# Kernel optimization log

Measured on AMD Instinct MI355X. Metric: run time of the kernel, lower is better.

## Reference

```python
import jax, jax.numpy as jnp
import numpy as np
import math

H = 16
LN_EPS = 1e-5


def setup_inputs() -> dict:
    key = jax.random.key(0)
    ks = jax.random.split(key, 12)
    D = 1024
    F = T = 2048
    S = 512
    inp = {
        "hidden_states": jax.random.normal(ks[0], (S, D), jnp.float32),
        "fpos": jax.random.randint(ks[1], (F,), 0, 512, jnp.int64 if jax.config.jax_enable_x64 else jnp.int32).astype(jnp.int32),
        "tpos": jax.random.randint(ks[2], (T,), 0, 512, jnp.int32),
        "Wq": jax.random.normal(ks[3], (D, D), jnp.float32) * 0.02,
        "Wk": jax.random.normal(ks[4], (D, D), jnp.float32) * 0.02,
        "Wcb": jax.random.normal(ks[5], (D, H), jnp.float32) * 0.02,
        "Wv": jax.random.normal(ks[6], (D, D), jnp.float32) * 0.02,
        "bv": jnp.zeros((D,), jnp.float32),
        "mixing": jax.random.normal(ks[7], (H, D), jnp.float32) * 0.2,
        "Wd": jax.random.normal(ks[8], (D, D), jnp.float32) * 0.02,
        "bd": jnp.zeros((D,), jnp.float32),
        "ln_gamma": jnp.ones((D,), jnp.float32),
        "ln_beta": jnp.zeros((D,), jnp.float32),
    }
    return inp


def reference(hidden_states, fpos, tpos, Wq, Wk, Wcb, Wv, bv, mixing, Wd, bd, ln_gamma, ln_beta):
    D = hidden_states.shape[-1]
    Dh = D // H
    scale = 1.0 / math.sqrt(D / H)  # attention_head_size = dim_key_query_all / num_heads

    fidx = fpos % 512
    tidx = tpos % 512
    from_seq = hidden_states[fidx]            # [F, D]
    to_seq = hidden_states[tidx]              # [T, D]

    q = from_seq @ Wq                          # [F, D]
    k = to_seq @ Wk                            # [T, D]

    # per-head query mixing: mixed_query[h, f, d] = q[f, d] * mixing[h, d]
    mixed_q = q[None, :, :] * mixing[:, None, :]          # [H, F, D]
    scores = jnp.einsum('hfd,td->hft', mixed_q, k)        # [H, F, T]

    # content bias: [T, H] -> broadcast over queries as [H, 1, T]
    cb = (to_seq @ Wcb).T                                 # [H, T]
    scores = (scores + cb[:, None, :]) * scale

    probs = jax.nn.softmax(scores, axis=-1)               # [H, F, T]

    v = (to_seq @ Wv + bv).reshape(-1, H, Dh).transpose(1, 0, 2)  # [H, T, Dh]
    ctx = jnp.matmul(probs, v)                             # [H, F, Dh]
    ctx = ctx.transpose(1, 0, 2).reshape(-1, D)            # [F, D]

    out = ctx @ Wd + bd                                    # [F, D]
    res = from_seq + out

    mu = jnp.mean(res, axis=-1, keepdims=True)
    var = jnp.var(res, axis=-1, keepdims=True)
    normed = (res - mu) / jnp.sqrt(var + LN_EPS)
    return normed * ln_gamma + ln_beta
```

## Files before the change

kernel.cpp:

```cpp
#include <hip/hip_runtime.h>
#include <stdint.h>
#include <math.h>

typedef float    f32x4 __attribute__((ext_vector_type(4)));
typedef float    f32x2 __attribute__((ext_vector_type(2)));
typedef short    s16x8 __attribute__((ext_vector_type(8)));
typedef short    s16x4 __attribute__((ext_vector_type(4)));
typedef unsigned u32x2 __attribute__((ext_vector_type(2)));

#define SCALE_LOG2E 0.1803368751839806f

__device__ __forceinline__ float bf2f(short s) {
  unsigned u = ((unsigned)(unsigned short)s) << 16;
  return __builtin_bit_cast(float, u);
}
__device__ __forceinline__ short f2bf(float f) {
  unsigned u = __builtin_bit_cast(unsigned, f);
  u = u + 0x7fffu + ((u >> 16) & 1u);
  return (short)(u >> 16);
}
__device__ __forceinline__ unsigned cvtpk(float lo, float hi) {
  unsigned r;
  asm("v_cvt_pk_bf16_f32 %0, %1, %2" : "=v"(r) : "v"(lo), "v"(hi));
  return r;
}
__device__ __forceinline__ void g2l16(const void* g, void* l) {
  __builtin_amdgcn_global_load_lds((const __attribute__((address_space(1))) void*)g,
                                   (__attribute__((address_space(3))) void*)l,
                                   16, 0, 0);
}
#define BARRIER() do { __builtin_amdgcn_s_barrier(); __builtin_amdgcn_sched_barrier(0); } while (0)
#define VMCNT(N)  asm volatile("s_waitcnt vmcnt(" #N ")" ::: "memory")
#define LGKM0()   do { asm volatile("s_waitcnt lgkmcnt(0)" ::: "memory"); __builtin_amdgcn_sched_barrier(0); } while (0)
#define MFMA(a, b, c)  __builtin_amdgcn_mfma_f32_16x16x32_bf16(a, b, c, 0, 0, 0)
#define MFMA8(a, b, c) __builtin_amdgcn_mfma_f32_16x16x32_fp8_fp8(a, b, c, 0, 0, 0)

__device__ __forceinline__ int pi32(int t) {
  return (t & ~31) | ((t & 15) << 1) | ((t >> 4) & 1);
}

__global__ void wtrans_kernel(const float* __restrict__ Wq, const float* __restrict__ Wk,
                              const float* __restrict__ Wv, const float* __restrict__ Wd,
                              short* __restrict__ WqT, short* __restrict__ WkT,
                              short* __restrict__ WvT, short* __restrict__ WdT) {
  __shared__ float tile[64][65];
  const float* src; short* dst;
  switch (blockIdx.z) {
    case 0: src = Wq; dst = WqT; break;
    case 1: src = Wk; dst = WkT; break;
    case 2: src = Wv; dst = WvT; break;
    default: src = Wd; dst = WdT; break;
  }
  int k0 = blockIdx.y * 64;
  int n0 = blockIdx.x * 64;
  int tid = threadIdx.x;
#pragma unroll
  for (int p = 0; p < 4; ++p) {
    int idx = p * 1024 + tid * 4;
    int r = idx >> 6, c = idx & 63;
    f32x4 v = *(const f32x4*)(src + (size_t)(k0 + r) * 1024 + n0 + c);
    tile[r][c + 0] = v[0]; tile[r][c + 1] = v[1];
    tile[r][c + 2] = v[2]; tile[r][c + 3] = v[3];
  }
  __syncthreads();
#pragma unroll
  for (int p = 0; p < 2; ++p) {
    int idx = p * 2048 + tid * 8;
    int r = idx >> 6, c = idx & 63;
    s16x8 o;
#pragma unroll
    for (int i = 0; i < 8; ++i) o[i] = f2bf(tile[c + i][r]);
    *(s16x8*)(dst + (size_t)(n0 + r) * 1024 + k0 + c) = o;
  }
}

__global__ void smallconv_kernel(const float* __restrict__ Wcb, const float* __restrict__ mixing,
                                 short* __restrict__ WcbT, short* __restrict__ mixbf) {
  int idx = blockIdx.x * 256 + threadIdx.x;
  if (idx < 16384) {
    int h = idx >> 10, d = idx & 1023;
    WcbT[idx] = f2bf(Wcb[d * 16 + h]);
  } else {
    int j = idx - 16384;
    mixbf[j] = f2bf(mixing[j] * (SCALE_LOG2E * 64.0f));
  }
}

__global__ void gather_kernel(const float* __restrict__ hidden, const int* __restrict__ fpos,
                              const int* __restrict__ tpos, float* __restrict__ from_f,
                              short* __restrict__ from_bf, short* __restrict__ to_bf) {
  int row = blockIdx.x;
  int c = threadIdx.x * 4;
  if (blockIdx.y == 0) {
    int src = fpos[row] & 511;
    f32x4 v = *(const f32x4*)(hidden + (size_t)src * 1024 + c);
    *(f32x4*)(from_f + (size_t)row * 1024 + c) = v;
    s16x4 o;
#pragma unroll
    for (int i = 0; i < 4; ++i) o[i] = f2bf(v[i]);
    *(s16x4*)(from_bf + (size_t)row * 1024 + c) = o;
  } else {
    int src = tpos[row] & 511;
    f32x4 v = *(const f32x4*)(hidden + (size_t)src * 1024 + c);
    s16x4 o;
#pragma unroll
    for (int i = 0; i < 4; ++i) o[i] = f2bf(v[i]);
    *(s16x4*)(to_bf + (size_t)row * 1024 + c) = o;
  }
}

__global__ __launch_bounds__(256, 2)
void qkv_gemm(const short* __restrict__ from_bf, const short* __restrict__ to_bf,
              const short* __restrict__ WqT, const short* __restrict__ WkT,
              const short* __restrict__ WvT, const float* __restrict__ bv,
              short* __restrict__ q_swz, short* __restrict__ k_swz, short* __restrict__ vTs) {
  __shared__ __align__(16) short As[128][64];
  __shared__ __align__(16) short Bs[128][64];
  int mode = blockIdx.z;
  const short* A = (mode == 0) ? from_bf : to_bf;
  const short* B = (mode == 0) ? WqT : (mode == 1) ? WkT : WvT;
  int m0 = blockIdx.x * 128, n0 = blockIdx.y * 128;
  int tid = threadIdx.x;
  int w = tid >> 6, l = tid & 63;
  int wr = w >> 1, wc = w & 1;
  f32x4 acc[4][4] = {};
  for (int k0 = 0; k0 < 1024; k0 += 64) {
    __syncthreads();
#pragma unroll
    for (int i = 0; i < 4; ++i) {
      int off = i * 4096 + tid * 16;
      int r = off >> 7, cb_ = off & 127;
      g2l16(A + ((size_t)(m0 + r) << 10) + k0 + (cb_ >> 1), (short*)As + (off >> 1));
      g2l16(B + ((size_t)(n0 + r) << 10) + k0 + (cb_ >> 1), (short*)Bs + (off >> 1));
    }
    __syncthreads();
#pragma unroll
    for (int ks = 0; ks < 2; ++ks) {
      s16x8 af[4], bfr[4];
#pragma unroll
      for (int m = 0; m < 4; ++m)
        af[m] = *(const s16x8*)&As[wr * 64 + m * 16 + (l & 15)][ks * 32 + (l >> 4) * 8];
#pragma unroll
      for (int n = 0; n < 4; ++n)
        bfr[n] = *(const s16x8*)&Bs[wc * 64 + n * 16 + (l & 15)][ks * 32 + (l >> 4) * 8];
#pragma unroll
      for (int m = 0; m < 4; ++m)
#pragma unroll
        for (int n = 0; n < 4; ++n)
          acc[m][n] = MFMA(af[m], bfr[n], acc[m][n]);
    }
  }
  int lr = (l >> 4) * 4, lc = l & 15;
#pragma unroll
  for (int m = 0; m < 4; ++m)
#pragma unroll
    for (int n = 0; n < 4; ++n) {
      int row = m0 + wr * 64 + m * 16 + lr;
      int col = n0 + wc * 64 + n * 16 + lc;
      if (mode == 0) {
#pragma unroll
        for (int r = 0; r < 4; ++r) {
          int rr = row + r;
          q_swz[(size_t)rr * 1024 + (col ^ ((rr & 7) << 3))] = f2bf(acc[m][n][r]);
        }
      } else if (mode == 1) {
#pragma unroll
        for (int r = 0; r < 4; ++r) {
          int rr = row + r;
          k_swz[(size_t)rr * 1024 + (col ^ ((rr & 7) << 3))] = f2bf(acc[m][n][r]);
        }
      } else {
        float b = bv[col];
#pragma unroll
        for (int r = 0; r < 4; ++r) {
          int rr = row + r;
          int tsw = pi32(rr) ^ ((col & 7) << 3);
          vTs[(size_t)col * 2048 + tsw] = f2bf(acc[m][n][r] + b);
        }
      }
    }
}

__global__ void k8_kernel(const short* __restrict__ k_swz, unsigned char* __restrict__ k8) {
  int gid = blockIdx.x * 256 + threadIdx.x;
  int row = gid >> 7, c = (gid & 127) * 8;
  s16x8 v = *(const s16x8*)(k_swz + ((size_t)row << 10) + c);
  unsigned lo = 0, hi = 0;
  lo = __builtin_amdgcn_cvt_pk_fp8_f32(bf2f(v[0]) * 4.f, bf2f(v[1]) * 4.f, lo, false);
  lo = __builtin_amdgcn_cvt_pk_fp8_f32(bf2f(v[2]) * 4.f, bf2f(v[3]) * 4.f, lo, true);
  hi = __builtin_amdgcn_cvt_pk_fp8_f32(bf2f(v[4]) * 4.f, bf2f(v[5]) * 4.f, hi, false);
  hi = __builtin_amdgcn_cvt_pk_fp8_f32(bf2f(v[6]) * 4.f, bf2f(v[7]) * 4.f, hi, true);
  u32x2 o; o[0] = lo; o[1] = hi;
  *(u32x2*)(k8 + ((size_t)row << 10) + c) = o;
}

__global__ void qmix8_kernel(const short* __restrict__ q_swz, const short* __restrict__ mixbf,
                             unsigned char* __restrict__ qm8) {
  int f = blockIdx.x, h = blockIdx.y;
  int c = threadIdx.x * 8;
  int fs = (f & 7) << 3;
  s16x8 qv = *(const s16x8*)(q_swz + ((size_t)f << 10) + c);
  s16x8 mv = *(const s16x8*)(mixbf + ((size_t)h << 10) + (c ^ fs));
  float p[8];
#pragma unroll
  for (int i = 0; i < 8; ++i) p[i] = bf2f(qv[i]) * bf2f(mv[i]);
  unsigned lo = 0, hi = 0;
  lo = __builtin_amdgcn_cvt_pk_fp8_f32(p[0], p[1], lo, false);
  lo = __builtin_amdgcn_cvt_pk_fp8_f32(p[2], p[3], lo, true);
  hi = __builtin_amdgcn_cvt_pk_fp8_f32(p[4], p[5], hi, false);
  hi = __builtin_amdgcn_cvt_pk_fp8_f32(p[6], p[7], hi, true);
  u32x2 o; o[0] = lo; o[1] = hi;
  *(u32x2*)(qm8 + (((size_t)h * 2048 + f) << 10) + c) = o;
}

__global__ void cb_kernel(const short* __restrict__ to_bf, const short* __restrict__ WcbT,
                          float* __restrict__ cbv) {
  __shared__ short Wl[16 * 1024];
  int tid = threadIdx.x;
  for (int i = tid; i < 2048; i += 256)
    ((s16x8*)Wl)[i] = ((const s16x8*)WcbT)[i];
  __syncthreads();
  int w = tid >> 6, l = tid & 63;
  int t = blockIdx.x * 4 + w;
  const s16x8* xr = (const s16x8*)(to_bf + ((size_t)t << 10) + l * 16);
  s16x8 x0 = xr[0], x1 = xr[1];
  float xf[16];
#pragma unroll
  for (int i = 0; i < 8; ++i) { xf[i] = bf2f(x0[i]); xf[8 + i] = bf2f(x1[i]); }
#pragma unroll
  for (int h = 0; h < 16; ++h) {
    const s16x8* wr_ = (const s16x8*)(Wl + h * 1024 + l * 16);
    s16x8 w0 = wr_[0], w1 = wr_[1];
    float acc = 0.f;
#pragma unroll
    for (int i = 0; i < 8; ++i) { acc += xf[i] * bf2f(w0[i]); acc += xf[8 + i] * bf2f(w1[i]); }
#pragma unroll
    for (int s = 32; s; s >>= 1) acc += __shfl_xor(acc, s);
    if (l == 0) cbv[(size_t)h * 2048 + t] = acc * SCALE_LOG2E;
  }
}

__global__ __launch_bounds__(512, 4)
void attn_kernel(const unsigned char* __restrict__ qm8, const unsigned char* __restrict__ k8,
                 const short* __restrict__ vTs, const float* __restrict__ cbg,
                 float* __restrict__ ctxp, f32x2* __restrict__ mlb) {
  __shared__ __align__(16) char smem[67584];
  char* qmA = smem;          char* qmB = smem + 16384;
  char* ktA = smem + 32768;  char* ktB = smem + 40960;
  char* vt  = smem + 49152;
  float* cbl = (float*)(smem + 65536);
  const int f0 = blockIdx.x * 256, h = blockIdx.y, ts = blockIdx.z;
  const int tb = ts << 9;
  const int tid = threadIdx.x, w = tid >> 6, l = tid & 63;
  const int lr = l >> 4, lc = l & 15;
  const int swz8 = (lc & 7) << 3;
  cbl[tid & 511] = cbg[h * 2048 + tb + (tid & 511)];
  const unsigned char* qbase = qm8 + (((size_t)h * 2048 + f0) << 10);

#define ISSUE_QK(qmb, ktb, k0e, trow0)                                                      \
  do {                                                                                      \
    _Pragma("unroll") for (int i_ = 0; i_ < 2; ++i_) {                                      \
      int off_ = i_ * 8192 + tid * 16;                                                      \
      g2l16(qbase + ((size_t)(off_ >> 6) << 10) + (k0e) + (off_ & 63), (qmb) + off_);       \
    }                                                                                       \
    {                                                                                       \
      int off_ = tid * 16;                                                                  \
      g2l16(k8 + ((size_t)((trow0) + (off_ >> 6)) << 10) + (k0e) + (off_ & 63),             \
            (ktb) + off_);                                                                  \
    }                                                                                       \
  } while (0)

  ISSUE_QK(qmA, ktA, 0, tb);

  float m_run[8], l_run[8];
#pragma unroll
  for (int s2 = 0; s2 < 8; ++s2) { m_run[s2] = -1e30f; l_run[s2] = 0.f; }
  f32x4 ctx[2][4] = {};

  for (int t0 = 0; t0 < 512; t0 += 128) {
#pragma unroll
    for (int i = 0; i < 2; ++i) {
      int off = i * 8192 + tid * 16;
      g2l16(vTs + (((size_t)(h * 64 + (off >> 8))) << 11) + tb + t0 + ((off & 255) >> 1),
            vt + off);
    }
    f32x4 sacc[2][8] = {};
    for (int c = 0; c < 16; ++c) {
      char* qmb = (c & 1) ? qmB : qmA;
      char* ktb = (c & 1) ? ktB : ktA;
      if (c < 15) {
        ISSUE_QK((c & 1) ? qmA : qmB, (c & 1) ? ktA : ktB, (c + 1) * 64, tb + t0);
      } else if (t0 < 384) {
        ISSUE_QK(qmA, ktA, 0, tb + t0 + 128);
      }
      if (c == 0) { VMCNT(5); }
      else if (c == 15 && t0 == 384) { VMCNT(0); }
      else { VMCNT(3); }
      BARRIER();
#pragma unroll
      for (int ks = 0; ks < 2; ++ks) {
        int xr = (ks * 32 + lr * 8) ^ swz8;
        long af0 = *(const long*)(qmb + ((w * 32 + lc) << 6) + xr);
        long af1 = *(const long*)(qmb + ((w * 32 + 16 + lc) << 6) + xr);
        __builtin_amdgcn_s_setprio(1);
#pragma unroll
        for (int n = 0; n < 8; ++n) {
          long bfr = *(const long*)(ktb + ((n * 16 + lc) << 6) + xr);
          sacc[0][n] = MFMA8(af0, bfr, sacc[0][n]);
          sacc[1][n] = MFMA8(af1, bfr, sacc[1][n]);
        }
        __builtin_amdgcn_s_setprio(0);
      }
      BARRIER();
    }
    float pm[8];
#pragma unroll
    for (int s2 = 0; s2 < 8; ++s2) pm[s2] = -1e30f;
#pragma unroll
    for (int m = 0; m < 2; ++m)
#pragma unroll
      for (int n = 0; n < 8; ++n) {
        float cbv = cbl[t0 + n * 16 + lc];
#pragma unroll
        for (int r = 0; r < 4; ++r) {
          float s = fmaf(sacc[m][n][r], 0.00390625f, cbv);
          sacc[m][n][r] = s;
          pm[m * 4 + r] = fmaxf(pm[m * 4 + r], s);
        }
      }
#pragma unroll
    for (int s_ = 1; s_ < 16; s_ <<= 1)
#pragma unroll
      for (int s2 = 0; s2 < 8; ++s2) pm[s2] = fmaxf(pm[s2], __shfl_xor(pm[s2], s_));
    float tsum[8];
#pragma unroll
    for (int s2 = 0; s2 < 8; ++s2) {
      float mnew = fmaxf(m_run[s2], pm[s2]);
      float corr = exp2f(m_run[s2] - mnew);
      m_run[s2] = mnew; l_run[s2] *= corr; tsum[s2] = 0.f;
      int m = s2 >> 2, r = s2 & 3;
#pragma unroll
      for (int n2 = 0; n2 < 4; ++n2) ctx[m][n2][r] *= corr;
    }
#pragma unroll
    for (int m = 0; m < 2; ++m)
#pragma unroll
      for (int n = 0; n < 8; ++n)
#pragma unroll
        for (int r = 0; r < 4; ++r) {
          float e = exp2f(sacc[m][n][r] - m_run[m * 4 + r]);
          sacc[m][n][r] = e;
          tsum[m * 4 + r] += e;
        }
#pragma unroll
    for (int s_ = 1; s_ < 16; s_ <<= 1)
#pragma unroll
      for (int s2 = 0; s2 < 8; ++s2) tsum[s2] += __shfl_xor(tsum[s2], s_);
#pragma unroll
    for (int s2 = 0; s2 < 8; ++s2) l_run[s2] += tsum[s2];
    char* ptw = qmB + (w << 11);
#pragma unroll
    for (int qq = 0; qq < 4; ++qq) {
      if (qq) { LGKM0(); }
#pragma unroll
      for (int m = 0; m < 2; ++m)
#pragma unroll
        for (int r = 0; r < 4; ++r) {
          int row = m * 16 + lr * 4 + r;
          unsigned pk = cvtpk(sacc[m][2 * qq][r], sacc[m][2 * qq + 1][r]);
          *(unsigned*)(ptw + (row << 6) + ((lc << 2) ^ ((row & 3) << 4))) = pk;
        }
      LGKM0();
      s16x8 paf0 = *(const s16x8*)(ptw + (lc << 6) + ((lr * 16) ^ ((lc & 3) << 4)));
      s16x8 paf1 = *(const s16x8*)(ptw + ((16 + lc) << 6) + ((lr * 16) ^ ((lc & 3) << 4)));
#pragma unroll
      for (int n2 = 0; n2 < 4; ++n2) {
        s16x8 vb = *(const s16x8*)(vt + ((n2 * 16 + lc) << 8) +
                                   ((qq * 64 + lr * 16) ^ ((lc & 7) << 4)));
        ctx[0][n2] = MFMA(paf0, vb, ctx[0][n2]);
        ctx[1][n2] = MFMA(paf1, vb, ctx[1][n2]);
      }
    }
    BARRIER();
  }
  const int pb = (h * 4 + ts) * 2048;
#pragma unroll
  for (int m = 0; m < 2; ++m)
#pragma unroll
    for (int n2 = 0; n2 < 4; ++n2)
#pragma unroll
      for (int r = 0; r < 4; ++r) {
        int f = f0 + w * 32 + m * 16 + lr * 4 + r;
        ctxp[((size_t)(pb + f) << 6) + n2 * 16 + lc] = ctx[m][n2][r];
      }
  if (lc == 0) {
#pragma unroll
    for (int s2 = 0; s2 < 8; ++s2) {
      int f = f0 + w * 32 + (s2 >> 2) * 16 + lr * 4 + (s2 & 3);
      f32x2 v; v[0] = m_run[s2]; v[1] = l_run[s2];
      mlb[pb + f] = v;
    }
  }
#undef ISSUE_QK
}

__global__ void combine_kernel(const float* __restrict__ ctxp, const f32x2* __restrict__ mlb,
                               short* __restrict__ ctx_bf) {
  int f = blockIdx.x, tid = threadIdx.x;
  int h = tid >> 4, d4 = (tid & 15) * 4;
  f32x2 ml[4];
  float mx = -1e30f;
#pragma unroll
  for (int p = 0; p < 4; ++p) {
    ml[p] = mlb[(h * 4 + p) * 2048 + f];
    mx = fmaxf(mx, ml[p][0]);
  }
  float e[4], L = 0.f;
#pragma unroll
  for (int p = 0; p < 4; ++p) { e[p] = exp2f(ml[p][0] - mx); L += ml[p][1] * e[p]; }
  float inv = 1.f / L;
  f32x4 s = {};
#pragma unroll
  for (int p = 0; p < 4; ++p) {
    f32x4 cp = *(const f32x4*)(ctxp + (((size_t)(h * 4 + p) * 2048 + f) << 6) + d4);
#pragma unroll
    for (int i = 0; i < 4; ++i) s[i] += cp[i] * e[p];
  }
  s16x4 o;
#pragma unroll
  for (int i = 0; i < 4; ++i) o[i] = f2bf(s[i] * inv);
  *(s16x4*)(ctx_bf + ((size_t)f << 10) + h * 64 + d4) = o;
}

__global__ __launch_bounds__(256, 2)
void gemm_out(const short* __restrict__ A, const short* __restrict__ B,
              const float* __restrict__ bias, const float* __restrict__ resid,
              float* __restrict__ Cout) {
  __shared__ __align__(16) short As[128][64];
  __shared__ __align__(16) short Bs[128][64];
  int m0 = blockIdx.x * 128, n0 = blockIdx.y * 128;
  int tid = threadIdx.x;
  int w = tid >> 6, l = tid & 63;
  int wr = w >> 1, wc = w & 1;
  f32x4 acc[4][4] = {};
  for (int k0 = 0; k0 < 1024; k0 += 64) {
    __syncthreads();
#pragma unroll
    for (int i = 0; i < 4; ++i) {
      int off = i * 4096 + tid * 16;
      int r = off >> 7, cb_ = off & 127;
      g2l16(A + ((size_t)(m0 + r) << 10) + k0 + (cb_ >> 1), (short*)As + (off >> 1));
      g2l16(B + ((size_t)(n0 + r) << 10) + k0 + (cb_ >> 1), (short*)Bs + (off >> 1));
    }
    __syncthreads();
#pragma unroll
    for (int ks = 0; ks < 2; ++ks) {
      s16x8 af[4], bfr[4];
#pragma unroll
      for (int m = 0; m < 4; ++m)
        af[m] = *(const s16x8*)&As[wr * 64 + m * 16 + (l & 15)][ks * 32 + (l >> 4) * 8];
#pragma unroll
      for (int n = 0; n < 4; ++n)
        bfr[n] = *(const s16x8*)&Bs[wc * 64 + n * 16 + (l & 15)][ks * 32 + (l >> 4) * 8];
#pragma unroll
      for (int m = 0; m < 4; ++m)
#pragma unroll
        for (int n = 0; n < 4; ++n)
          acc[m][n] = MFMA(af[m], bfr[n], acc[m][n]);
    }
  }
  int lr = (l >> 4) * 4, lc = l & 15;
#pragma unroll
  for (int m = 0; m < 4; ++m)
#pragma unroll
    for (int n = 0; n < 4; ++n) {
      int row = m0 + wr * 64 + m * 16 + lr;
      int col = n0 + wc * 64 + n * 16 + lc;
      float b = bias[col];
#pragma unroll
      for (int r = 0; r < 4; ++r)
        Cout[(size_t)(row + r) * 1024 + col] = acc[m][n][r] + b + resid[(size_t)(row + r) * 1024 + col];
    }
}

__global__ void ln_kernel(const float* __restrict__ res, const float* __restrict__ gamma,
                          const float* __restrict__ beta, float* __restrict__ out) {
  int row = blockIdx.x, tid = threadIdx.x;
  f32x4 x = *(const f32x4*)(res + ((size_t)row << 10) + tid * 4);
  float s = x[0] + x[1] + x[2] + x[3];
  float s2 = x[0] * x[0] + x[1] * x[1] + x[2] * x[2] + x[3] * x[3];
#pragma unroll
  for (int m = 1; m < 64; m <<= 1) { s += __shfl_xor(s, m); s2 += __shfl_xor(s2, m); }
  __shared__ float red[8];
  int w = tid >> 6, l = tid & 63;
  if (l == 0) { red[w] = s; red[4 + w] = s2; }
  __syncthreads();
  s = red[0] + red[1] + red[2] + red[3];
  s2 = red[4] + red[5] + red[6] + red[7];
  float mu = s * (1.f / 1024.f);
  float var = s2 * (1.f / 1024.f) - mu * mu;
  float rstd = rsqrtf(var + 1e-5f);
  f32x4 o;
#pragma unroll
  for (int i = 0; i < 4; ++i)
    o[i] = (x[i] - mu) * rstd * gamma[tid * 4 + i] + beta[tid * 4 + i];
  *(f32x4*)(out + ((size_t)row << 10) + tid * 4) = o;
}

extern "C" void kernel_launch(void* const* d_in, const int* in_sizes, int n_in,
                              void* d_out, int out_size, void* d_ws, size_t ws_size,
                              hipStream_t stream) {
  const float* hidden = (const float*)d_in[0];
  const int*   fpos   = (const int*)d_in[1];
  const int*   tpos   = (const int*)d_in[2];
  const float* Wq     = (const float*)d_in[3];
  const float* Wk     = (const float*)d_in[4];
  const float* Wcb    = (const float*)d_in[5];
  const float* Wv     = (const float*)d_in[6];
  const float* bv     = (const float*)d_in[7];
  const float* mixing = (const float*)d_in[8];
  const float* Wd     = (const float*)d_in[9];
  const float* bd     = (const float*)d_in[10];
  const float* gamma  = (const float*)d_in[11];
  const float* beta   = (const float*)d_in[12];

  char* p = (char*)d_ws;
  auto alloc = [&](size_t bytes) { char* r = p; p += (bytes + 255) & ~(size_t)255; return r; };
  float* from_f  = (float*)alloc((size_t)2048 * 1024 * 4);
  short* from_bf = (short*)alloc((size_t)2048 * 1024 * 2);
  short* to_bf   = (short*)alloc((size_t)2048 * 1024 * 2);
  short* WqT     = (short*)alloc((size_t)1024 * 1024 * 2);
  short* WkT     = (short*)alloc((size_t)1024 * 1024 * 2);
  short* WvT     = (short*)alloc((size_t)1024 * 1024 * 2);
  short* WdT     = (short*)alloc((size_t)1024 * 1024 * 2);
  short* WcbT    = (short*)alloc((size_t)16 * 1024 * 2);
  short* mixbf   = (short*)alloc((size_t)16 * 1024 * 2);
  short* q_swz   = (short*)alloc((size_t)2048 * 1024 * 2);
  short* k_swz   = (short*)alloc((size_t)2048 * 1024 * 2);
  short* vTs     = (short*)alloc((size_t)1024 * 2048 * 2);
  unsigned char* k8  = (unsigned char*)alloc((size_t)2048 * 1024);
  unsigned char* qm8 = (unsigned char*)alloc((size_t)16 * 2048 * 1024);
  float* cbb     = (float*)alloc((size_t)16 * 2048 * 4);
  short* ctx_bf  = (short*)alloc((size_t)2048 * 1024 * 2);
  float* ctxp    = (float*)alloc((size_t)64 * 2048 * 64 * 4);
  f32x2* mlb     = (f32x2*)alloc((size_t)64 * 2048 * 8);

  wtrans_kernel<<<dim3(16, 16, 4), 256, 0, stream>>>(Wq, Wk, Wv, Wd, WqT, WkT, WvT, WdT);
  smallconv_kernel<<<128, 256, 0, stream>>>(Wcb, mixing, WcbT, mixbf);
  gather_kernel<<<dim3(2048, 2), 256, 0, stream>>>(hidden, fpos, tpos, from_f, from_bf, to_bf);
  qkv_gemm<<<dim3(16, 8, 3), 256, 0, stream>>>(from_bf, to_bf, WqT, WkT, WvT, bv,
                                               q_swz, k_swz, vTs);
  k8_kernel<<<1024, 256, 0, stream>>>(k_swz, k8);
  cb_kernel<<<512, 256, 0, stream>>>(to_bf, WcbT, cbb);
  qmix8_kernel<<<dim3(2048, 16), 128, 0, stream>>>(q_swz, mixbf, qm8);
  attn_kernel<<<dim3(8, 16, 4), 512, 0, stream>>>(qm8, k8, vTs, cbb, ctxp, mlb);
  combine_kernel<<<2048, 256, 0, stream>>>(ctxp, mlb, ctx_bf);
  gemm_out<<<dim3(16, 8), 256, 0, stream>>>(ctx_bf, WdT, bd, from_f, (float*)d_out);
  ln_kernel<<<2048, 256, 0, stream>>>((float*)d_out, gamma, beta, (float*)d_out);
}
```

Measured before the change: 393.8 us.

## Retile attention to 128-query blocks with 2-way key split and wider K chunks

The attention kernel now processes 128 queries per block (16 per wave) across 2 key splits of 1024 instead of 256 queries across 4 splits of 512. It loads 128-byte K chunks per stage with a new 16-row XOR swizzle, and that swizzle moves into the fp8 conversion kernels. The content bias is read straight into registers instead of staged in shared memory, and the combine step merges only 2 partials. The aim is fewer partial outputs and less combine traffic, with longer MFMA inner loops per barrier, at the cost of more LDS per block and lower occupancy (launch bound 2).

Result: faster. 349.5 us (-11.2%).

```diff
diff --git a/kernel.cpp b/kernel.cpp
--- a/kernel.cpp
+++ b/kernel.cpp
@@ -113,7 +113,7 @@
 void qkv_gemm(const short* __restrict__ from_bf, const short* __restrict__ to_bf,
               const short* __restrict__ WqT, const short* __restrict__ WkT,
               const short* __restrict__ WvT, const float* __restrict__ bv,
-              short* __restrict__ q_swz, short* __restrict__ k_swz, short* __restrict__ vTs) {
+              short* __restrict__ q_bf, short* __restrict__ k_bf, short* __restrict__ vTs) {
   __shared__ __align__(16) short As[128][64];
   __shared__ __align__(16) short Bs[128][64];
   int mode = blockIdx.z;
@@ -159,16 +159,10 @@
       int col = n0 + wc * 64 + n * 16 + lc;
       if (mode == 0) {
 #pragma unroll
-        for (int r = 0; r < 4; ++r) {
-          int rr = row + r;
-          q_swz[(size_t)rr * 1024 + (col ^ ((rr & 7) << 3))] = f2bf(acc[m][n][r]);
-        }
+        for (int r = 0; r < 4; ++r) q_bf[(size_t)(row + r) * 1024 + col] = f2bf(acc[m][n][r]);
       } else if (mode == 1) {
 #pragma unroll
-        for (int r = 0; r < 4; ++r) {
-          int rr = row + r;
-          k_swz[(size_t)rr * 1024 + (col ^ ((rr & 7) << 3))] = f2bf(acc[m][n][r]);
-        }
+        for (int r = 0; r < 4; ++r) k_bf[(size_t)(row + r) * 1024 + col] = f2bf(acc[m][n][r]);
       } else {
         float b = bv[col];
 #pragma unroll
@@ -181,26 +175,25 @@
     }
 }
 
-__global__ void k8_kernel(const short* __restrict__ k_swz, unsigned char* __restrict__ k8) {
+__global__ void k8_kernel(const short* __restrict__ k_bf, unsigned char* __restrict__ k8) {
   int gid = blockIdx.x * 256 + threadIdx.x;
   int row = gid >> 7, c = (gid & 127) * 8;
-  s16x8 v = *(const s16x8*)(k_swz + ((size_t)row << 10) + c);
+  s16x8 v = *(const s16x8*)(k_bf + ((size_t)row << 10) + c);
   unsigned lo = 0, hi = 0;
   lo = __builtin_amdgcn_cvt_pk_fp8_f32(bf2f(v[0]) * 4.f, bf2f(v[1]) * 4.f, lo, false);
   lo = __builtin_amdgcn_cvt_pk_fp8_f32(bf2f(v[2]) * 4.f, bf2f(v[3]) * 4.f, lo, true);
   hi = __builtin_amdgcn_cvt_pk_fp8_f32(bf2f(v[4]) * 4.f, bf2f(v[5]) * 4.f, hi, false);
   hi = __builtin_amdgcn_cvt_pk_fp8_f32(bf2f(v[6]) * 4.f, bf2f(v[7]) * 4.f, hi, true);
   u32x2 o; o[0] = lo; o[1] = hi;
-  *(u32x2*)(k8 + ((size_t)row << 10) + c) = o;
-}
-
-__global__ void qmix8_kernel(const short* __restrict__ q_swz, const short* __restrict__ mixbf,
+  *(u32x2*)(k8 + ((size_t)row << 10) + (c ^ ((row & 15) << 3))) = o;
+}
+
+__global__ void qmix8_kernel(const short* __restrict__ q_bf, const short* __restrict__ mixbf,
                              unsigned char* __restrict__ qm8) {
   int f = blockIdx.x, h = blockIdx.y;
   int c = threadIdx.x * 8;
-  int fs = (f & 7) << 3;
-  s16x8 qv = *(const s16x8*)(q_swz + ((size_t)f << 10) + c);
-  s16x8 mv = *(const s16x8*)(mixbf + ((size_t)h << 10) + (c ^ fs));
+  s16x8 qv = *(const s16x8*)(q_bf + ((size_t)f << 10) + c);
+  s16x8 mv = *(const s16x8*)(mixbf + ((size_t)h << 10) + c);
   float p[8];
 #pragma unroll
   for (int i = 0; i < 8; ++i) p[i] = bf2f(qv[i]) * bf2f(mv[i]);
@@ -210,7 +203,7 @@
   hi = __builtin_amdgcn_cvt_pk_fp8_f32(p[4], p[5], hi, false);
   hi = __builtin_amdgcn_cvt_pk_fp8_f32(p[6], p[7], hi, true);
   u32x2 o; o[0] = lo; o[1] = hi;
-  *(u32x2*)(qm8 + (((size_t)h * 2048 + f) << 10) + c) = o;
+  *(u32x2*)(qm8 + (((size_t)h * 2048 + f) << 10) + (c ^ ((f & 15) << 3))) = o;
 }
 
 __global__ void cb_kernel(const short* __restrict__ to_bf, const short* __restrict__ WcbT,
@@ -240,163 +233,146 @@
   }
 }
 
-__global__ __launch_bounds__(512, 4)
+__global__ __launch_bounds__(512, 2)
 void attn_kernel(const unsigned char* __restrict__ qm8, const unsigned char* __restrict__ k8,
                  const short* __restrict__ vTs, const float* __restrict__ cbg,
                  float* __restrict__ ctxp, f32x2* __restrict__ mlb) {
-  __shared__ __align__(16) char smem[67584];
+  __shared__ __align__(16) char smem[81920];
   char* qmA = smem;          char* qmB = smem + 16384;
-  char* ktA = smem + 32768;  char* ktB = smem + 40960;
-  char* vt  = smem + 49152;
-  float* cbl = (float*)(smem + 65536);
-  const int f0 = blockIdx.x * 256, h = blockIdx.y, ts = blockIdx.z;
-  const int tb = ts << 9;
+  char* ktA = smem + 32768;  char* ktB = smem + 49152;
+  char* vt  = smem + 65536;
+  const int f0 = blockIdx.x * 128, h = blockIdx.y, ts = blockIdx.z;
+  const int tb = ts << 10;
   const int tid = threadIdx.x, w = tid >> 6, l = tid & 63;
   const int lr = l >> 4, lc = l & 15;
-  const int swz8 = (lc & 7) << 3;
-  cbl[tid & 511] = cbg[h * 2048 + tb + (tid & 511)];
   const unsigned char* qbase = qm8 + (((size_t)h * 2048 + f0) << 10);
 
-#define ISSUE_QK(qmb, ktb, k0e, trow0)                                                      \
-  do {                                                                                      \
-    _Pragma("unroll") for (int i_ = 0; i_ < 2; ++i_) {                                      \
-      int off_ = i_ * 8192 + tid * 16;                                                      \
-      g2l16(qbase + ((size_t)(off_ >> 6) << 10) + (k0e) + (off_ & 63), (qmb) + off_);       \
-    }                                                                                       \
-    {                                                                                       \
-      int off_ = tid * 16;                                                                  \
-      g2l16(k8 + ((size_t)((trow0) + (off_ >> 6)) << 10) + (k0e) + (off_ & 63),             \
-            (ktb) + off_);                                                                  \
-    }                                                                                       \
+#define ISSUE_QK(qmb, ktb, kc, trow0)                                                     \
+  do {                                                                                    \
+    _Pragma("unroll") for (int i_ = 0; i_ < 2; ++i_) {                                    \
+      int off_ = i_ * 8192 + tid * 16;                                                    \
+      g2l16(qbase + ((size_t)(off_ >> 7) << 10) + (kc) + (off_ & 127), (qmb) + off_);     \
+    }                                                                                     \
+    _Pragma("unroll") for (int i_ = 0; i_ < 2; ++i_) {                                    \
+      int off_ = i_ * 8192 + tid * 16;                                                    \
+      g2l16(k8 + ((size_t)((trow0) + (off_ >> 7)) << 10) + (kc) + (off_ & 127),           \
+            (ktb) + off_);                                                                \
+    }                                                                                     \
   } while (0)
 
   ISSUE_QK(qmA, ktA, 0, tb);
 
-  float m_run[8], l_run[8];
-#pragma unroll
-  for (int s2 = 0; s2 < 8; ++s2) { m_run[s2] = -1e30f; l_run[s2] = 0.f; }
-  f32x4 ctx[2][4] = {};
-
-  for (int t0 = 0; t0 < 512; t0 += 128) {
+  float m_run[4], l_run[4];
+#pragma unroll
+  for (int s2 = 0; s2 < 4; ++s2) { m_run[s2] = -1e30f; l_run[s2] = 0.f; }
+  f32x4 ctx[4] = {};
+
+  for (int t0 = 0; t0 < 1024; t0 += 128) {
 #pragma unroll
     for (int i = 0; i < 2; ++i) {
       int off = i * 8192 + tid * 16;
-      g2l16(vTs + (((size_t)(h * 64 + (off >> 8))) << 11) + tb + t0 + ((off & 255) >> 1),
+      g2l16(vTs + ((size_t)(h * 64 + (off >> 8)) << 11) + tb + t0 + ((off & 255) >> 1),
             vt + off);
     }
-    f32x4 sacc[2][8] = {};
-    for (int c = 0; c < 16; ++c) {
+    float cbr[8];
+#pragma unroll
+    for (int n = 0; n < 8; ++n) cbr[n] = cbg[h * 2048 + tb + t0 + n * 16 + lc];
+    f32x4 sacc[8] = {};
+    for (int c = 0; c < 8; ++c) {
       char* qmb = (c & 1) ? qmB : qmA;
       char* ktb = (c & 1) ? ktB : ktA;
-      if (c < 15) {
-        ISSUE_QK((c & 1) ? qmA : qmB, (c & 1) ? ktA : ktB, (c + 1) * 64, tb + t0);
-      } else if (t0 < 384) {
+      if (c < 7) {
+        ISSUE_QK((c & 1) ? qmA : qmB, (c & 1) ? ktA : ktB, (c + 1) * 128, tb + t0);
+      } else if (t0 < 896) {
         ISSUE_QK(qmA, ktA, 0, tb + t0 + 128);
       }
-      if (c == 0) { VMCNT(5); }
-      else if (c == 15 && t0 == 384) { VMCNT(0); }
-      else { VMCNT(3); }
+      if (c == 0) { VMCNT(14); }
+      else if (c == 7 && t0 == 896) { VMCNT(0); }
+      else { VMCNT(4); }
       BARRIER();
 #pragma unroll
-      for (int ks = 0; ks < 2; ++ks) {
-        int xr = (ks * 32 + lr * 8) ^ swz8;
-        long af0 = *(const long*)(qmb + ((w * 32 + lc) << 6) + xr);
-        long af1 = *(const long*)(qmb + ((w * 32 + 16 + lc) << 6) + xr);
+      for (int s = 0; s < 4; ++s) {
+        int xr = (s * 32 + lr * 8) ^ (lc << 3);
+        long af = *(const long*)(qmb + ((w * 16 + lc) << 7) + xr);
         __builtin_amdgcn_s_setprio(1);
 #pragma unroll
         for (int n = 0; n < 8; ++n) {
-          long bfr = *(const long*)(ktb + ((n * 16 + lc) << 6) + xr);
-          sacc[0][n] = MFMA8(af0, bfr, sacc[0][n]);
-          sacc[1][n] = MFMA8(af1, bfr, sacc[1][n]);
+          long bfr = *(const long*)(ktb + ((n * 16 + lc) << 7) + xr);
+          sacc[n] = MFMA8(af, bfr, sacc[n]);
         }
         __builtin_amdgcn_s_setprio(0);
       }
       BARRIER();
     }
-    float pm[8];
-#pragma unroll
-    for (int s2 = 0; s2 < 8; ++s2) pm[s2] = -1e30f;
-#pragma unroll
-    for (int m = 0; m < 2; ++m)
-#pragma unroll
-      for (int n = 0; n < 8; ++n) {
-        float cbv = cbl[t0 + n * 16 + lc];
-#pragma unroll
-        for (int r = 0; r < 4; ++r) {
-          float s = fmaf(sacc[m][n][r], 0.00390625f, cbv);
-          sacc[m][n][r] = s;
-          pm[m * 4 + r] = fmaxf(pm[m * 4 + r], s);
-        }
+    float pm[4] = {-1e30f, -1e30f, -1e30f, -1e30f};
+#pragma unroll
+    for (int n = 0; n < 8; ++n)
+#pragma unroll
+      for (int r = 0; r < 4; ++r) {
+        float s = fmaf(sacc[n][r], 0.00390625f, cbr[n]);
+        sacc[n][r] = s;
+        pm[r] = fmaxf(pm[r], s);
       }
 #pragma unroll
     for (int s_ = 1; s_ < 16; s_ <<= 1)
 #pragma unroll
-      for (int s2 = 0; s2 < 8; ++s2) pm[s2] = fmaxf(pm[s2], __shfl_xor(pm[s2], s_));
-    float tsum[8];
-#pragma unroll
-    for (int s2 = 0; s2 < 8; ++s2) {
-      float mnew = fmaxf(m_run[s2], pm[s2]);
-      float corr = exp2f(m_run[s2] - mnew);
-      m_run[s2] = mnew; l_run[s2] *= corr; tsum[s2] = 0.f;
-      int m = s2 >> 2, r = s2 & 3;
-#pragma unroll
-      for (int n2 = 0; n2 < 4; ++n2) ctx[m][n2][r] *= corr;
-    }
-#pragma unroll
-    for (int m = 0; m < 2; ++m)
-#pragma unroll
-      for (int n = 0; n < 8; ++n)
-#pragma unroll
-        for (int r = 0; r < 4; ++r) {
-          float e = exp2f(sacc[m][n][r] - m_run[m * 4 + r]);
-          sacc[m][n][r] = e;
-          tsum[m * 4 + r] += e;
-        }
+      for (int r = 0; r < 4; ++r) pm[r] = fmaxf(pm[r], __shfl_xor(pm[r], s_));
+    float tsum[4];
+#pragma unroll
+    for (int r = 0; r < 4; ++r) {
+      float mnew = fmaxf(m_run[r], pm[r]);
+      float corr = exp2f(m_run[r] - mnew);
+      m_run[r] = mnew; l_run[r] *= corr; tsum[r] = 0.f;
+#pragma unroll
+      for (int n2 = 0; n2 < 4; ++n2) ctx[n2][r] *= corr;
+    }
+#pragma unroll
+    for (int n = 0; n < 8; ++n)
+#pragma unroll
+      for (int r = 0; r < 4; ++r) {
+        float e = exp2f(sacc[n][r] - m_run[r]);
+        sacc[n][r] = e;
+        tsum[r] += e;
+      }
 #pragma unroll
     for (int s_ = 1; s_ < 16; s_ <<= 1)
 #pragma unroll
-      for (int s2 = 0; s2 < 8; ++s2) tsum[s2] += __shfl_xor(tsum[s2], s_);
-#pragma unroll
-    for (int s2 = 0; s2 < 8; ++s2) l_run[s2] += tsum[s2];
-    char* ptw = qmB + (w << 11);
+      for (int r = 0; r < 4; ++r) tsum[r] += __shfl_xor(tsum[r], s_);
+#pragma unroll
+    for (int r = 0; r < 4; ++r) l_run[r] += tsum[r];
+    char* ptw = qmB + (w << 10);
 #pragma unroll
     for (int qq = 0; qq < 4; ++qq) {
       if (qq) { LGKM0(); }
 #pragma unroll
-      for (int m = 0; m < 2; ++m)
-#pragma unroll
-        for (int r = 0; r < 4; ++r) {
-          int row = m * 16 + lr * 4 + r;
-          unsigned pk = cvtpk(sacc[m][2 * qq][r], sacc[m][2 * qq + 1][r]);
-          *(unsigned*)(ptw + (row << 6) + ((lc << 2) ^ ((row & 3) << 4))) = pk;
-        }
+      for (int r = 0; r < 4; ++r) {
+        int row = lr * 4 + r;
+        unsigned pk = cvtpk(sacc[2 * qq][r], sacc[2 * qq + 1][r]);
+        *(unsigned*)(ptw + (row << 6) + ((lc ^ (r << 2)) << 2)) = pk;
+      }
       LGKM0();
-      s16x8 paf0 = *(const s16x8*)(ptw + (lc << 6) + ((lr * 16) ^ ((lc & 3) << 4)));
-      s16x8 paf1 = *(const s16x8*)(ptw + ((16 + lc) << 6) + ((lr * 16) ^ ((lc & 3) << 4)));
+      s16x8 paf = *(const s16x8*)(ptw + (lc << 6) + ((lr * 16) ^ ((lc & 3) << 4)));
 #pragma unroll
       for (int n2 = 0; n2 < 4; ++n2) {
         s16x8 vb = *(const s16x8*)(vt + ((n2 * 16 + lc) << 8) +
                                    ((qq * 64 + lr * 16) ^ ((lc & 7) << 4)));
-        ctx[0][n2] = MFMA(paf0, vb, ctx[0][n2]);
-        ctx[1][n2] = MFMA(paf1, vb, ctx[1][n2]);
+        ctx[n2] = MFMA(paf, vb, ctx[n2]);
       }
     }
     BARRIER();
   }
-  const int pb = (h * 4 + ts) * 2048;
-#pragma unroll
-  for (int m = 0; m < 2; ++m)
-#pragma unroll
-    for (int n2 = 0; n2 < 4; ++n2)
-#pragma unroll
-      for (int r = 0; r < 4; ++r) {
-        int f = f0 + w * 32 + m * 16 + lr * 4 + r;
-        ctxp[((size_t)(pb + f) << 6) + n2 * 16 + lc] = ctx[m][n2][r];
-      }
+  const int pb = (h * 2 + ts) * 2048;
+#pragma unroll
+  for (int n2 = 0; n2 < 4; ++n2)
+#pragma unroll
+    for (int r = 0; r < 4; ++r) {
+      int f = f0 + w * 16 + lr * 4 + r;
+      ctxp[((size_t)(pb + f) << 6) + n2 * 16 + lc] = ctx[n2][r];
+    }
   if (lc == 0) {
 #pragma unroll
-    for (int s2 = 0; s2 < 8; ++s2) {
-      int f = f0 + w * 32 + (s2 >> 2) * 16 + lr * 4 + (s2 & 3);
+    for (int s2 = 0; s2 < 4; ++s2) {
+      int f = f0 + w * 16 + lr * 4 + s2;
       f32x2 v; v[0] = m_run[s2]; v[1] = l_run[s2];
       mlb[pb + f] = v;
     }
@@ -408,27 +384,16 @@
                                short* __restrict__ ctx_bf) {
   int f = blockIdx.x, tid = threadIdx.x;
   int h = tid >> 4, d4 = (tid & 15) * 4;
-  f32x2 ml[4];
-  float mx = -1e30f;
-#pragma unroll
-  for (int p = 0; p < 4; ++p) {
-    ml[p] = mlb[(h * 4 + p) * 2048 + f];
-    mx = fmaxf(mx, ml[p][0]);
-  }
-  float e[4], L = 0.f;
-#pragma unroll
-  for (int p = 0; p < 4; ++p) { e[p] = exp2f(ml[p][0] - mx); L += ml[p][1] * e[p]; }
-  float inv = 1.f / L;
-  f32x4 s = {};
-#pragma unroll
-  for (int p = 0; p < 4; ++p) {
-    f32x4 cp = *(const f32x4*)(ctxp + (((size_t)(h * 4 + p) * 2048 + f) << 6) + d4);
-#pragma unroll
-    for (int i = 0; i < 4; ++i) s[i] += cp[i] * e[p];
-  }
+  f32x2 a = mlb[(h * 2 + 0) * 2048 + f];
+  f32x2 b = mlb[(h * 2 + 1) * 2048 + f];
+  float m = fmaxf(a[0], b[0]);
+  float e0 = exp2f(a[0] - m), e1 = exp2f(b[0] - m);
+  float inv = 1.f / (a[1] * e0 + b[1] * e1);
+  f32x4 c0 = *(const f32x4*)(ctxp + (((size_t)(h * 2 + 0) * 2048 + f) << 6) + d4);
+  f32x4 c1 = *(const f32x4*)(ctxp + (((size_t)(h * 2 + 1) * 2048 + f) << 6) + d4);
   s16x4 o;
 #pragma unroll
-  for (int i = 0; i < 4; ++i) o[i] = f2bf(s[i] * inv);
+  for (int i = 0; i < 4; ++i) o[i] = f2bf((c0[i] * e0 + c1[i] * e1) * inv);
   *(s16x4*)(ctx_bf + ((size_t)f << 10) + h * 64 + d4) = o;
 }
 
@@ -535,25 +500,25 @@
   short* WdT     = (short*)alloc((size_t)1024 * 1024 * 2);
   short* WcbT    = (short*)alloc((size_t)16 * 1024 * 2);
   short* mixbf   = (short*)alloc((size_t)16 * 1024 * 2);
-  short* q_swz   = (short*)alloc((size_t)2048 * 1024 * 2);
-  short* k_swz   = (short*)alloc((size_t)2048 * 1024 * 2);
+  short* q_bf    = (short*)alloc((size_t)2048 * 1024 * 2);
+  short* k_bf    = (short*)alloc((size_t)2048 * 1024 * 2);
   short* vTs     = (short*)alloc((size_t)1024 * 2048 * 2);
   unsigned char* k8  = (unsigned char*)alloc((size_t)2048 * 1024);
   unsigned char* qm8 = (unsigned char*)alloc((size_t)16 * 2048 * 1024);
   float* cbb     = (float*)alloc((size_t)16 * 2048 * 4);
   short* ctx_bf  = (short*)alloc((size_t)2048 * 1024 * 2);
-  float* ctxp    = (float*)alloc((size_t)64 * 2048 * 64 * 4);
-  f32x2* mlb     = (f32x2*)alloc((size_t)64 * 2048 * 8);
+  float* ctxp    = (float*)alloc((size_t)32 * 2048 * 64 * 4);
+  f32x2* mlb     = (f32x2*)alloc((size_t)32 * 2048 * 8);
 
   wtrans_kernel<<<dim3(16, 16, 4), 256, 0, stream>>>(Wq, Wk, Wv, Wd, WqT, WkT, WvT, WdT);
   smallconv_kernel<<<128, 256, 0, stream>>>(Wcb, mixing, WcbT, mixbf);
   gather_kernel<<<dim3(2048, 2), 256, 0, stream>>>(hidden, fpos, tpos, from_f, from_bf, to_bf);
   qkv_gemm<<<dim3(16, 8, 3), 256, 0, stream>>>(from_bf, to_bf, WqT, WkT, WvT, bv,
-                                               q_swz, k_swz, vTs);
-  k8_kernel<<<1024, 256, 0, stream>>>(k_swz, k8);
+                                               q_bf, k_bf, vTs);
+  k8_kernel<<<1024, 256, 0, stream>>>(k_bf, k8);
   cb_kernel<<<512, 256, 0, stream>>>(to_bf, WcbT, cbb);
-  qmix8_kernel<<<dim3(2048, 16), 128, 0, stream>>>(q_swz, mixbf, qm8);
-  attn_kernel<<<dim3(8, 16, 4), 512, 0, stream>>>(qm8, k8, vTs, cbb, ctxp, mlb);
+  qmix8_kernel<<<dim3(2048, 16), 128, 0, stream>>>(q_bf, mixbf, qm8);
+  attn_kernel<<<dim3(16, 16, 2), 512, 0, stream>>>(qm8, k8, vTs, cbb, ctxp, mlb);
   combine_kernel<<<2048, 256, 0, stream>>>(ctxp, mlb, ctx_bf);
   gemm_out<<<dim3(16, 8), 256, 0, stream>>>(ctx_bf, WdT, bd, from_f, (float*)d_out);
   ln_kernel<<<2048, 256, 0, stream>>>((float*)d_out, gamma, beta, (float*)d_out);
```
